# Optimization experiments

Measured on AMD Instinct MI355X. Metric: run time of the kernel, lower is better.

The kernel has to match this reference:

```python
import jax, jax.numpy as jnp
import numpy as np

B, F, H = 16384, 2048, 4096   # batch, n_features, n_hidden
D, K = 4096, 2048             # num_of_demos, num_of_features


def setup_inputs() -> dict:
    key = jax.random.key(0)
    ks = jax.random.split(key, 16)
    s = 0.02
    return {
        "x": jax.random.normal(ks[0], (B, F), jnp.float32),
        "demo_metric": jax.random.uniform(ks[1], (D, K), jnp.float32),
        "alpha": jax.random.normal(ks[2], (K,), jnp.float32),
        "sample_loss": jax.random.uniform(ks[3], (D, K), jnp.float32),
        "subdom_constant": jax.random.uniform(ks[4], (1,), jnp.float32),
        "num_of_demos": D,
        "num_of_features": K,
        "W1": jax.random.normal(ks[5], (F, H), jnp.float32) * s,
        "b1": jnp.zeros((H,), jnp.float32),
        "W2": jax.random.normal(ks[6], (H, H), jnp.float32) * s,
        "b2": jnp.zeros((H,), jnp.float32),
        "W3": jax.random.normal(ks[7], (H, H), jnp.float32) * s,
        "b3": jnp.zeros((H,), jnp.float32),
        "W4": jax.random.normal(ks[8], (H, 2), jnp.float32) * s,
        "b4": jnp.zeros((2,), jnp.float32),
    }


def reference(x, demo_metric, alpha, sample_loss, subdom_constant,
              num_of_demos, num_of_features,
              W1, b1, W2, b2, W3, b3, W4, b4):
    # subdom hinge loss: max(alpha_k * (sample_loss_jk - demo_loss_jk) + 1, 0) - c
    margin = alpha[None, :] * (sample_loss - demo_metric) + 1.0  # [D, K]
    subdom = jnp.maximum(margin, 0.0) - subdom_constant          # broadcast c
    loss = jnp.sum(subdom)

    # MLP classifier (dropout = identity at inference) + sigmoid
    h = jax.nn.relu(x @ W1 + b1)
    h = jax.nn.relu(h @ W2 + b2)
    h = jax.nn.relu(h @ W3 + b3)
    probs = jax.nn.sigmoid(h @ W4 + b4)  # [B, 2]
    return (loss, probs)
```

## Files before the change

kernel.cpp:

```cpp
#include <hip/hip_runtime.h>
#include <cstdint>
#include <cstddef>

typedef unsigned short u16;
typedef __attribute__((ext_vector_type(8))) __bf16 bf16x8;
typedef __attribute__((ext_vector_type(4))) float f32x4;

__device__ __forceinline__ u16 f2bf(float f) {
  union { float f; unsigned u; } v; v.f = f;
  unsigned r = v.u + 0x7FFFu + ((v.u >> 16) & 1u);
  return (u16)(r >> 16);
}
__device__ __forceinline__ float bf2f(unsigned h) {
  union { unsigned u; float f; } v; v.u = h << 16;
  return v.f;
}

__global__ void init_loss_kernel(const float* __restrict__ c,
                                 const int* __restrict__ D,
                                 const int* __restrict__ K,
                                 float* __restrict__ out) {
  out[0] = -c[0] * (float)D[0] * (float)K[0];
}

__global__ void subdom_kernel(const float4* __restrict__ dm,
                              const float4* __restrict__ sl,
                              const float4* __restrict__ alpha4,
                              float* __restrict__ out, int n4, int k4mask) {
  const int stride = gridDim.x * blockDim.x;
  float s = 0.f;
  for (int i = blockIdx.x * blockDim.x + threadIdx.x; i < n4; i += stride) {
    float4 d = dm[i], l = sl[i], a = alpha4[i & k4mask];
    s += fmaxf(fmaf(a.x, l.x - d.x, 1.f), 0.f);
    s += fmaxf(fmaf(a.y, l.y - d.y, 1.f), 0.f);
    s += fmaxf(fmaf(a.z, l.z - d.z, 1.f), 0.f);
    s += fmaxf(fmaf(a.w, l.w - d.w, 1.f), 0.f);
  }
#pragma unroll
  for (int off = 32; off > 0; off >>= 1) s += __shfl_down(s, off, 64);
  __shared__ float red[4];
  const int lane = threadIdx.x & 63, wave = threadIdx.x >> 6;
  if (lane == 0) red[wave] = s;
  __syncthreads();
  if (threadIdx.x == 0) atomicAdd(out, red[0] + red[1] + red[2] + red[3]);
}

__global__ void cast_f32_bf16_kernel(const float4* __restrict__ in,
                                     u16* __restrict__ out, int n4) {
  const int stride = gridDim.x * blockDim.x;
  for (int i = blockIdx.x * blockDim.x + threadIdx.x; i < n4; i += stride) {
    float4 v = in[i];
    uint2 p;
    p.x = (unsigned)f2bf(v.x) | ((unsigned)f2bf(v.y) << 16);
    p.y = (unsigned)f2bf(v.z) | ((unsigned)f2bf(v.w) << 16);
    ((uint2*)out)[i] = p;
  }
}

__global__ void transpose_cast_kernel(const float* __restrict__ in,
                                      u16* __restrict__ out, int K, int N) {
  __shared__ float tile[32][33];
  const int bx = blockIdx.x * 32;
  const int by = blockIdx.y * 32;
  const int tx = threadIdx.x, ty = threadIdx.y;
#pragma unroll
  for (int i = ty; i < 32; i += 8)
    tile[i][tx] = in[(size_t)(by + i) * N + bx + tx];
  __syncthreads();
#pragma unroll
  for (int i = ty; i < 32; i += 8)
    out[(size_t)(bx + i) * K + by + tx] = f2bf(tile[tx][i]);
}


__device__ __forceinline__ void gload_lds16(const void* g, void* l) {
  __builtin_amdgcn_global_load_lds(
      (const __attribute__((address_space(1))) void*)g,
      (__attribute__((address_space(3))) void*)l, 16, 0, 0);
}

#define VMW(N) asm volatile("s_waitcnt vmcnt(" #N ")" ::: "memory")
#define MF(a, b, c) __builtin_amdgcn_mfma_f32_16x16x32_bf16(a, b, c, 0, 0, 0)

#define STAGE_A(BU, Q, TK)                                                    \
  gload_lds16(A + aGbase + (size_t)((Q)*64) * K + (size_t)(TK)*64,            \
              (void*)(As + ((BU)*4 + (Q)) * 4096 + swave))

#define STAGE_B(BU, NH, HH, TK)                                               \
  gload_lds16(Bt + bGbase + (size_t)((NH)*32 + (HH)*128) * K +                \
                  (size_t)(TK)*64,                                            \
              (void*)(Bs + ((BU)*2 + (NH)) * 8192 + (HH)*4096 + swave))

#define ARD(BU, MH)                                                           \
  {                                                                           \
    const u16* Ar_ = As + ((BU)*4 + wm2 + (MH)) * 4096 + abase;               \
    _Pragma("unroll") for (int f_ = 0; f_ < 4; ++f_) {                        \
      af0[f_] = *(const bf16x8*)(Ar_ + f_ * 1024 + aslot0);                   \
      af1[f_] = *(const bf16x8*)(Ar_ + f_ * 1024 + aslot1);                   \
    }                                                                         \
  }

#define BRD(BF, BU, NH2)                                                      \
  {                                                                           \
    const u16* Br_ = Bs + ((BU)*2 + (NH2)) * 8192 + bbase;                    \
    BF[0] = *(const bf16x8*)(Br_ + aslot0);                                   \
    BF[1] = *(const bf16x8*)(Br_ + aslot1);                                   \
    BF[2] = *(const bf16x8*)(Br_ + 1024 + aslot0);                            \
    BF[3] = *(const bf16x8*)(Br_ + 1024 + aslot1);                            \
  }

#define MFMA32(MH)                                                            \
  __builtin_amdgcn_s_setprio(1);                                              \
  _Pragma("unroll") for (int f_ = 0; f_ < 4; ++f_) {                          \
    acc[(MH)*4 + f_][0] = MF(af0[f_], bfr0[0], acc[(MH)*4 + f_][0]);          \
    acc[(MH)*4 + f_][0] = MF(af1[f_], bfr0[1], acc[(MH)*4 + f_][0]);          \
    acc[(MH)*4 + f_][1] = MF(af0[f_], bfr0[2], acc[(MH)*4 + f_][1]);          \
    acc[(MH)*4 + f_][1] = MF(af1[f_], bfr0[3], acc[(MH)*4 + f_][1]);          \
    acc[(MH)*4 + f_][2] = MF(af0[f_], bfr1[0], acc[(MH)*4 + f_][2]);          \
    acc[(MH)*4 + f_][2] = MF(af1[f_], bfr1[1], acc[(MH)*4 + f_][2]);          \
    acc[(MH)*4 + f_][3] = MF(af0[f_], bfr1[2], acc[(MH)*4 + f_][3]);          \
    acc[(MH)*4 + f_][3] = MF(af1[f_], bfr1[3], acc[(MH)*4 + f_][3]);          \
  }                                                                           \
  __builtin_amdgcn_s_setprio(0);

__global__ __launch_bounds__(512, 2) void gemm256(
    const u16* __restrict__ A, const u16* __restrict__ Bt,
    const float* __restrict__ bias, u16* __restrict__ C,
    int M, int N, int K, int act) {
  __shared__ __align__(16) u16 As[2 * 4 * 4096];
  __shared__ __align__(16) u16 Bs[2 * 2 * 8192];

  const int gx = gridDim.x;
  const int bid = blockIdx.x + blockIdx.y * gx;
  const int cpx = (gx * gridDim.y) >> 3;
  const int tilei = (bid & 7) * cpx + (bid >> 3);
  const int m0 = (tilei / gx) * 256;
  const int n0 = (tilei % gx) * 256;

  const int tid = threadIdx.x;
  const int wave = tid >> 6, lane = tid & 63;
  const int l15 = lane & 15, quad = lane >> 4;
  const int wm = wave >> 2, wn = wave & 3;
  const int wm2 = wm << 1;
  const int lsw = l15 & 7;

  const int aslot0 = ((quad ^ lsw) << 3);
  const int aslot1 = (((4 + quad) ^ lsw) << 3);
  const int abase = l15 * 64;
  const int bbase = (wn * 32 + l15) * 64;

  const int srow = tid >> 3;
  const int skch = ((tid & 7) ^ (srow & 7)) << 3;
  const int brow = ((srow >> 5) << 6) + (srow & 31);
  const size_t aGbase = (size_t)(m0 + srow) * K + skch;
  const size_t bGbase = (size_t)(n0 + brow) * K + skch;
  const int swave = wave * 512;

  f32x4 acc[8][4];
#pragma unroll
  for (int i = 0; i < 8; ++i)
#pragma unroll
    for (int j = 0; j < 4; ++j) acc[i][j] = (f32x4){0.f, 0.f, 0.f, 0.f};
  bf16x8 af0[4], af1[4], bfr0[4], bfr1[4];

  STAGE_A(0, 0, 0); STAGE_A(0, 2, 0);
  STAGE_B(0, 0, 0, 0); STAGE_B(0, 0, 1, 0);
  STAGE_B(0, 1, 0, 0); STAGE_B(0, 1, 1, 0);
  STAGE_A(0, 1, 0); STAGE_A(0, 3, 0);
  STAGE_B(1, 0, 0, 1); STAGE_B(1, 0, 1, 1);
  STAGE_B(1, 1, 0, 1); STAGE_B(1, 1, 1, 1);
  VMW(6);
  __builtin_amdgcn_s_barrier();

  const int niter = K >> 7;
  for (int it = 0; it < niter; ++it) {
    const int t1 = 2 * it + 1, t2 = 2 * it + 2, t3 = 2 * it + 3;
    const bool nl = (it + 1 < niter);
    BRD(bfr0, 0, 0);
    ARD(0, 0);
    BRD(bfr1, 0, 1);
    STAGE_A(1, 0, t1); STAGE_A(1, 2, t1);
    STAGE_A(1, 1, t1); STAGE_A(1, 3, t1);
    MFMA32(0);
    VMW(8);
    __builtin_amdgcn_s_barrier();
    ARD(0, 1);
    MFMA32(1);
    VMW(0);
    __builtin_amdgcn_s_barrier();
    BRD(bfr0, 1, 0);
    ARD(1, 0);
    BRD(bfr1, 1, 1);
    if (nl) {
      STAGE_B(0, 0, 0, t2); STAGE_B(0, 0, 1, t2);
      STAGE_B(0, 1, 0, t2); STAGE_B(0, 1, 1, t2);
      STAGE_A(0, 0, t2); STAGE_A(0, 2, t2);
    }
    MFMA32(0);
    __builtin_amdgcn_s_barrier();
    ARD(1, 1);
    if (nl) {
      STAGE_A(0, 1, t2); STAGE_A(0, 3, t2);
      STAGE_B(1, 0, 0, t3); STAGE_B(1, 0, 1, t3);
      STAGE_B(1, 1, 0, t3); STAGE_B(1, 1, 1, t3);
    }
    MFMA32(1);
    VMW(6);
    __builtin_amdgcn_s_barrier();
  }

#pragma unroll
  for (int mi = 0; mi < 8; ++mi) {
    const int row = m0 + wm * 128 + (mi >> 2) * 64 + (mi & 3) * 16 + quad * 4;
#pragma unroll
    for (int j = 0; j < 4; ++j) {
      const int col = n0 + wn * 64 + j * 16 + l15;
      const float bv = bias[col];
#pragma unroll
      for (int r = 0; r < 4; ++r) {
        float v = acc[mi][j][r] + bv;
        if (act) v = fmaxf(v, 0.f);
        C[(size_t)(row + r) * N + col] = f2bf(v);
      }
    }
  }
}

__global__ __launch_bounds__(256) void head_kernel(
    const u16* __restrict__ h, const float2* __restrict__ W4,
    const float* __restrict__ b4, float* __restrict__ out, int H) {
  const int row = blockIdx.x;
  const u16* hr = h + (size_t)row * H;
  const int tid = threadIdx.x;
  float p0 = 0.f, p1 = 0.f;
#pragma unroll
  for (int ii = 0; ii < 2; ++ii) {
    const int base = tid * 16 + ii * 8;
    const uint4 hv = *(const uint4*)(hr + base);
    const unsigned uu[4] = {hv.x, hv.y, hv.z, hv.w};
#pragma unroll
    for (int j = 0; j < 4; ++j) {
      float a0 = bf2f(uu[j] & 0xffffu);
      float a1 = bf2f(uu[j] >> 16);
      float2 w0 = W4[base + 2 * j];
      float2 w1 = W4[base + 2 * j + 1];
      p0 += a0 * w0.x + a1 * w1.x;
      p1 += a0 * w0.y + a1 * w1.y;
    }
  }
#pragma unroll
  for (int off = 32; off > 0; off >>= 1) {
    p0 += __shfl_down(p0, off, 64);
    p1 += __shfl_down(p1, off, 64);
  }
  __shared__ float r0[4], r1[4];
  const int lane = tid & 63, wave = tid >> 6;
  if (lane == 0) { r0[wave] = p0; r1[wave] = p1; }
  __syncthreads();
  if (tid == 0) {
    float l0 = r0[0] + r0[1] + r0[2] + r0[3] + b4[0];
    float l1 = r1[0] + r1[1] + r1[2] + r1[3] + b4[1];
    out[1 + row * 2] = 1.f / (1.f + __expf(-l0));
    out[2 + row * 2] = 1.f / (1.f + __expf(-l1));
  }
}

extern "C" void kernel_launch(void* const* d_in, const int* in_sizes, int n_in,
                              void* d_out, int out_size, void* d_ws,
                              size_t ws_size, hipStream_t stream) {
  (void)in_sizes; (void)n_in; (void)out_size; (void)ws_size;
  const float* x  = (const float*)d_in[0];
  const float* dm = (const float*)d_in[1];
  const float* al = (const float*)d_in[2];
  const float* sl = (const float*)d_in[3];
  const float* sc = (const float*)d_in[4];
  const int*   nd = (const int*)d_in[5];
  const int*   nf = (const int*)d_in[6];
  const float* W1 = (const float*)d_in[7];
  const float* b1 = (const float*)d_in[8];
  const float* W2 = (const float*)d_in[9];
  const float* b2 = (const float*)d_in[10];
  const float* W3 = (const float*)d_in[11];
  const float* b3 = (const float*)d_in[12];
  const float* W4 = (const float*)d_in[13];
  const float* b4 = (const float*)d_in[14];
  float* out = (float*)d_out;

  const int B = 16384, F = 2048, H = 4096, D = 4096, K = 2048;

  char* ws = (char*)d_ws;
  u16* xb = (u16*)ws;
  u16* wt = (u16*)(ws + (size_t)B * F * 2);
  u16* hA = (u16*)(ws + (size_t)B * F * 2 + (size_t)H * H * 2);
  u16* hB = hA + (size_t)B * H;

  init_loss_kernel<<<1, 1, 0, stream>>>(sc, nd, nf, out);
  subdom_kernel<<<1024, 256, 0, stream>>>((const float4*)dm, (const float4*)sl,
                                          (const float4*)al, out, D * K / 4,
                                          K / 4 - 1);
  cast_f32_bf16_kernel<<<4096, 256, 0, stream>>>((const float4*)x, xb, B * F / 4);
  transpose_cast_kernel<<<dim3(H / 32, F / 32), dim3(32, 8), 0, stream>>>(W1, wt, F, H);
  gemm256<<<dim3(H / 256, B / 256), 512, 0, stream>>>(xb, wt, b1, hA, B, H, F, 1);
  transpose_cast_kernel<<<dim3(H / 32, H / 32), dim3(32, 8), 0, stream>>>(W2, wt, H, H);
  gemm256<<<dim3(H / 256, B / 256), 512, 0, stream>>>(hA, wt, b2, hB, B, H, H, 1);
  transpose_cast_kernel<<<dim3(H / 32, H / 32), dim3(32, 8), 0, stream>>>(W3, wt, H, H);
  gemm256<<<dim3(H / 256, B / 256), 512, 0, stream>>>(hB, wt, b3, hA, B, H, H, 1);
  head_kernel<<<B, 256, 0, stream>>>(hA, (const float2*)W4, b4, out, H);
}
```

Baseline: 1.529 ms.

## Simplify GEMM main loop to whole-tile double buffering with one barrier per phase

Replaces the finely interleaved staging schedule, where A and B halves of different K-tiles were prefetched at staggered points with partial vmcnt waits, with a simple double-buffer scheme. Each phase now issues the entire next tile's global-to-LDS loads up front, computes on the current buffer, then waits for all loads and synchronizes once. This cuts the barrier count and the waitcnt bookkeeping, but prefetch depth drops to one tile and every phase ends with a full vmcnt(0) drain, so load latency may be exposed more.

```diff
diff --git a/kernel.cpp b/kernel.cpp
--- a/kernel.cpp
+++ b/kernel.cpp
@@ -90,6 +90,14 @@
   gload_lds16(Bt + bGbase + (size_t)((NH)*32 + (HH)*128) * K +                \
                   (size_t)(TK)*64,                                            \
               (void*)(Bs + ((BU)*2 + (NH)) * 8192 + (HH)*4096 + swave))
+
+#define STAGE_TILE(BU, TK)                                                    \
+  do {                                                                        \
+    STAGE_A(BU, 0, TK); STAGE_A(BU, 2, TK);                                   \
+    STAGE_B(BU, 0, 0, TK); STAGE_B(BU, 0, 1, TK);                             \
+    STAGE_B(BU, 1, 0, TK); STAGE_B(BU, 1, 1, TK);                             \
+    STAGE_A(BU, 1, TK); STAGE_A(BU, 3, TK);                                   \
+  } while (0)
 
 #define ARD(BU, MH)                                                           \
   {                                                                           \
@@ -123,6 +131,19 @@
   }                                                                           \
   __builtin_amdgcn_s_setprio(0);
 
+#define MEGAPHASE(BUF, SC)                                                    \
+  {                                                                           \
+    SC;                                                                       \
+    BRD(bfr0, BUF, 0);                                                        \
+    ARD(BUF, 0);                                                              \
+    BRD(bfr1, BUF, 1);                                                        \
+    MFMA32(0);                                                                \
+    ARD(BUF, 1);                                                              \
+    MFMA32(1);                                                                \
+    VMW(0);                                                                   \
+    __builtin_amdgcn_s_barrier();                                             \
+  }
+
 __global__ __launch_bounds__(512, 2) void gemm256(
     const u16* __restrict__ A, const u16* __restrict__ Bt,
     const float* __restrict__ bias, u16* __restrict__ C,
@@ -163,50 +184,16 @@
     for (int j = 0; j < 4; ++j) acc[i][j] = (f32x4){0.f, 0.f, 0.f, 0.f};
   bf16x8 af0[4], af1[4], bfr0[4], bfr1[4];
 
-  STAGE_A(0, 0, 0); STAGE_A(0, 2, 0);
-  STAGE_B(0, 0, 0, 0); STAGE_B(0, 0, 1, 0);
-  STAGE_B(0, 1, 0, 0); STAGE_B(0, 1, 1, 0);
-  STAGE_A(0, 1, 0); STAGE_A(0, 3, 0);
-  STAGE_B(1, 0, 0, 1); STAGE_B(1, 0, 1, 1);
-  STAGE_B(1, 1, 0, 1); STAGE_B(1, 1, 1, 1);
-  VMW(6);
+  STAGE_TILE(0, 0);
+  VMW(0);
   __builtin_amdgcn_s_barrier();
 
   const int niter = K >> 7;
   for (int it = 0; it < niter; ++it) {
-    const int t1 = 2 * it + 1, t2 = 2 * it + 2, t3 = 2 * it + 3;
+    const int t1 = 2 * it + 1, t2 = 2 * it + 2;
     const bool nl = (it + 1 < niter);
-    BRD(bfr0, 0, 0);
-    ARD(0, 0);
-    BRD(bfr1, 0, 1);
-    STAGE_A(1, 0, t1); STAGE_A(1, 2, t1);
-    STAGE_A(1, 1, t1); STAGE_A(1, 3, t1);
-    MFMA32(0);
-    VMW(8);
-    __builtin_amdgcn_s_barrier();
-    ARD(0, 1);
-    MFMA32(1);
-    VMW(0);
-    __builtin_amdgcn_s_barrier();
-    BRD(bfr0, 1, 0);
-    ARD(1, 0);
-    BRD(bfr1, 1, 1);
-    if (nl) {
-      STAGE_B(0, 0, 0, t2); STAGE_B(0, 0, 1, t2);
-      STAGE_B(0, 1, 0, t2); STAGE_B(0, 1, 1, t2);
-      STAGE_A(0, 0, t2); STAGE_A(0, 2, t2);
-    }
-    MFMA32(0);
-    __builtin_amdgcn_s_barrier();
-    ARD(1, 1);
-    if (nl) {
-      STAGE_A(0, 1, t2); STAGE_A(0, 3, t2);
-      STAGE_B(1, 0, 0, t3); STAGE_B(1, 0, 1, t3);
-      STAGE_B(1, 1, 0, t3); STAGE_B(1, 1, 1, t3);
-    }
-    MFMA32(1);
-    VMW(6);
-    __builtin_amdgcn_s_barrier();
+    MEGAPHASE(0, { STAGE_TILE(1, t1); });
+    MEGAPHASE(1, { if (nl) STAGE_TILE(0, t2); });
   }
 
 #pragma unroll
```

Result: slower. 1.908 ms (+24.7%).
